# Kernel tuning notes

Hardware: AMD Instinct MI355X
Metric: run time of the kernel (lower is better)

## Reference

```python
import jax, jax.numpy as jnp
import numpy as np

BN_EPS = 1e-5


def gcn_conv(x, src, dst, n, W, b):
    # PyG GCNConv: h = x @ W; add self-loops; symmetric deg^{-1/2} norm; scatter-add; + bias
    h = x @ W
    sl = jnp.arange(n, dtype=src.dtype)
    src_f = jnp.concatenate([src, sl])
    dst_f = jnp.concatenate([dst, sl])
    deg = jax.ops.segment_sum(jnp.ones_like(dst_f, dtype=h.dtype), dst_f, num_segments=n)
    dis = jnp.where(deg > 0, jax.lax.rsqrt(jnp.maximum(deg, 1.0)), 0.0)
    norm = dis[src_f] * dis[dst_f]                       # [E+N]
    msg = h[src_f] * norm[:, None]                       # gather + scale
    out = jax.ops.segment_sum(msg, dst_f, num_segments=n)  # scatter-add
    return out + b


def batchnorm(x, g, b):
    # training-mode BatchNorm1d (batch statistics), deterministic
    mu = jnp.mean(x, axis=0)
    var = jnp.mean((x - mu) ** 2, axis=0)
    return g * (x - mu) * jax.lax.rsqrt(var + BN_EPS) + b


def setup_inputs() -> dict:
    key = jax.random.key(0)
    ks = jax.random.split(key, 12)
    N, E, F_IN, D, M, G = 40000, 640000, 128, 128, 256, 2000
    x = jax.random.normal(ks[0], (N, F_IN), dtype=jnp.float32)
    edge_index = jax.random.randint(ks[1], (2, E), 0, N, dtype=jnp.int64)
    batch = jnp.sort(jax.random.randint(ks[2], (N,), 0, G, dtype=jnp.int64))
    s = lambda fi: 1.0 / np.sqrt(fi)
    W1 = jax.random.normal(ks[3], (F_IN, D), dtype=jnp.float32) * s(F_IN)
    b1 = jnp.zeros((D,), jnp.float32)
    W2 = jax.random.normal(ks[4], (D, D), dtype=jnp.float32) * s(D)
    b2 = jnp.zeros((D,), jnp.float32)
    bn1_g = jnp.ones((D,), jnp.float32); bn1_b = jnp.zeros((D,), jnp.float32)
    bn2_g = jnp.ones((D,), jnp.float32); bn2_b = jnp.zeros((D,), jnp.float32)
    fc1_w = jax.random.normal(ks[5], (D, M), dtype=jnp.float32) * s(D)
    fc1_b = jnp.zeros((M,), jnp.float32)
    fc2_w = jax.random.normal(ks[6], (M, M), dtype=jnp.float32) * s(M)
    fc2_b = jnp.zeros((M,), jnp.float32)
    fc3_w = jax.random.normal(ks[7], (M, 1), dtype=jnp.float32) * s(M)
    fc3_b = jnp.zeros((1,), jnp.float32)
    return dict(x=x, edge_index=edge_index, batch=batch, num_graphs=G,
                W1=W1, b1=b1, W2=W2, b2=b2,
                bn1_g=bn1_g, bn1_b=bn1_b, bn2_g=bn2_g, bn2_b=bn2_b,
                fc1_w=fc1_w, fc1_b=fc1_b, fc2_w=fc2_w, fc2_b=fc2_b,
                fc3_w=fc3_w, fc3_b=fc3_b)


def reference(x, edge_index, batch, num_graphs, W1, b1, W2, b2,
              bn1_g, bn1_b, bn2_g, bn2_b,
              fc1_w, fc1_b, fc2_w, fc2_b, fc3_w, fc3_b):
    n = x.shape[0]
    src, dst = edge_index[0], edge_index[1]
    h = gcn_conv(x, src, dst, n, W1, b1)
    h = jax.nn.relu(batchnorm(h, bn1_g, bn1_b))
    h = gcn_conv(h, src, dst, n, W2, b2)
    h = jax.nn.relu(batchnorm(h, bn2_g, bn2_b))
    g = jax.ops.segment_sum(h, batch, num_segments=num_graphs)  # scatter_sum pooling [G, D]
    g = jax.nn.relu(g @ fc1_w + fc1_b)   # dropout is identity in eval
    g = jax.nn.relu(g @ fc2_w + fc2_b)
    return g @ fc3_w + fc3_b             # [G, 1]
```

## Files before the change

### kernel.cpp

```cpp
#include <hip/hip_runtime.h>
#include <hip/hip_fp16.h>

#define NN 40000
#define NE 640000
#define DF 128
#define NG 2000
#define NCH 157
#define CNTB 625
#define GT_BLKS 625
#define NDPAD 40192

typedef unsigned int u32;
typedef __attribute__((ext_vector_type(8))) short short8;
typedef __attribute__((ext_vector_type(4))) float floatx4;

__device__ inline float2 bf2_to_f2(u32 u) {
    return make_float2(__uint_as_float(u << 16), __uint_as_float(u & 0xffff0000u));
}
__device__ inline u32 f_to_bf(float f) {
    u32 u = __float_as_uint(f);
    return (u + 0x7fffu + ((u >> 16) & 1u)) >> 16;
}
__device__ inline u32 pack_bf2(float a, float b) {
    return f_to_bf(a) | (f_to_bf(b) << 16);
}
__device__ inline float bf_to_f(short s) {
    return __uint_as_float(((u32)(unsigned short)s) << 16);
}
__device__ inline float colw_to_f(int cw) {
    return __half2float(__ushort_as_half((unsigned short)((u32)cw >> 16)));
}

template<bool BF16IN, bool FUSE_BN>
__device__ __forceinline__ void gemm_core(const void* __restrict__ Xv, const unsigned short* __restrict__ wt,
                                          u32* __restrict__ outb, const float* __restrict__ slots,
                                          const float* __restrict__ gam, const float* __restrict__ bet,
                                          int bid, char* sbuf, float* sc, float* sh) {
    unsigned short* wlds = (unsigned short*)sbuf;
    unsigned short* clds = (unsigned short*)sbuf;
    int tid = threadIdx.x;
    int row0 = bid * 64;

    if (FUSE_BN) {
        if (tid < 128) {
            float s = 0.f, q = 0.f;
            for (int k = 0; k < 64; k++) {
                s += slots[k * 256 + tid];
                q += slots[k * 256 + 128 + tid];
            }
            const float inv_n = 1.0f / (float)NN;
            float mu = s * inv_n;
            float va = fmaf(-mu, mu, q * inv_n);
            float a = gam[tid] * rsqrtf(va + 1e-5f);
            sc[tid] = a;
            sh[tid] = fmaf(-mu, a, bet[tid]);
        }
    }
    for (int i = tid; i < 2048; i += 256) {
        int c = i >> 4, s = i & 15;
        *(uint4*)&wlds[c * 128 + ((s ^ (c & 7)) << 3)] = ((const uint4*)wt)[i];
    }
    __syncthreads();

    int lane = tid & 63;
    int wave = tid >> 6;
    int qr = lane >> 4;
    int rl = lane & 15;

    int rA = row0 + wave * 16 + rl;
    floatx4 acc[8];
#pragma unroll
    for (int b = 0; b < 8; b++) acc[b] = (floatx4){0.f, 0.f, 0.f, 0.f};
#pragma unroll
    for (int kb = 0; kb < 4; kb++) {
        int k0 = kb * 32 + qr * 8;
        short8 a0;
        if (!BF16IN) {
            const float* p0 = (const float*)Xv + (size_t)rA * DF + k0;
            float4 u0 = *(const float4*)p0, u1 = *(const float4*)(p0 + 4);
            float fa[8] = {u0.x, u0.y, u0.z, u0.w, u1.x, u1.y, u1.z, u1.w};
#pragma unroll
            for (int j = 0; j < 8; j++) a0[j] = (short)f_to_bf(fa[j]);
        } else {
            a0 = *(const short8*)((const u32*)Xv + (size_t)rA * 64 + (k0 >> 1));
            if (FUSE_BN) {
#pragma unroll
                for (int j = 0; j < 8; j++) {
                    float f0 = fmaxf(fmaf(bf_to_f(a0[j]), sc[k0 + j], sh[k0 + j]), 0.f);
                    a0[j] = (short)f_to_bf(f0);
                }
            }
        }
#pragma unroll
        for (int ct = 0; ct < 8; ct++) {
            int rowB = ct * 16 + rl;
            short8 bfr = *(const short8*)&wlds[rowB * 128 + ((((kb << 2) + qr) ^ (rl & 7)) << 3)];
            acc[ct] = __builtin_amdgcn_mfma_f32_16x16x32_bf16(a0, bfr, acc[ct], 0, 0, 0);
        }
    }
    __syncthreads();
#pragma unroll
    for (int ct = 0; ct < 8; ct++)
#pragma unroll
        for (int r = 0; r < 4; r++) {
            int lr = wave * 16 + qr * 4 + r;
            int c = ct * 16 + rl;
            clds[lr * 128 + (((c >> 3) ^ (lr & 7)) << 3) + (c & 7)] = (unsigned short)f_to_bf(acc[ct][r]);
        }
    __syncthreads();
    for (int i = tid; i < 1024; i += 256) {
        int lr = i >> 4, s = i & 15;
        uint4 v = *(const uint4*)&clds[lr * 128 + ((s ^ (lr & 7)) << 3)];
        ((uint4*)(outb + (size_t)(row0 + lr) * 64))[s] = v;
    }
}

__global__ __launch_bounds__(256) void k_prep(const float* __restrict__ W1, const float* __restrict__ W2,
                                              unsigned short* __restrict__ wt1, unsigned short* __restrict__ wt2,
                                              float* __restrict__ slots0, int* __restrict__ deg) {
    int bid = blockIdx.x, tid = threadIdx.x;
    if (bid < 64) {
        slots0[bid * 512 + tid] = 0.f;
        slots0[bid * 512 + 256 + tid] = 0.f;
    } else if (bid < 104) {
        int i = (bid - 64) * 1024 + tid;
#pragma unroll
        for (int q = 0; q < 4; q++) {
            int j = i + q * 256;
            if (j < NDPAD) deg[j] = 0;
        }
    } else if (bid < 168) {
        int i = (bid - 104) * 256 + tid;
        wt1[i] = (unsigned short)f_to_bf(W1[(i & 127) * 128 + (i >> 7)]);
    } else {
        int i = (bid - 168) * 256 + tid;
        wt2[i] = (unsigned short)f_to_bf(W2[(i & 127) * 128 + (i >> 7)]);
    }
}

__global__ __launch_bounds__(256, 5) void k_countgemm(const int* __restrict__ dst,
                                                      int* __restrict__ deg,
                                                      const unsigned short* __restrict__ wt1,
                                                      const float* __restrict__ X, u32* __restrict__ outb) {
    __shared__ __align__(16) char sbuf[32768];
    int bid = blockIdx.x;
    int tid = threadIdx.x;
    if (bid < CNTB) {
        int i4 = bid * 256 + tid;
        int4 d4 = ((const int4*)dst)[i4];
        atomicAdd(&deg[d4.x], 1);
        atomicAdd(&deg[d4.y], 1);
        atomicAdd(&deg[d4.z], 1);
        atomicAdd(&deg[d4.w], 1);
        return;
    }
    gemm_core<false, false>(X, wt1, outb, nullptr, nullptr, nullptr,
                            bid - CNTB, sbuf, nullptr, nullptr);
}

__global__ __launch_bounds__(256) void k_scan(const int* __restrict__ deg,
                                              int* __restrict__ row_ptr, int* __restrict__ curs,
                                              float* __restrict__ dis) {
    __shared__ int red[256];
    __shared__ int ls[256];
    int tid = threadIdx.x;
    int wnd = blockIdx.x;
    int part = 0;
    int lim = wnd * 256;
    for (int idx = tid; idx < lim; idx += 256) part += deg[idx];
    red[tid] = part;
    int n = lim + tid;
    int d = deg[n];
    ls[tid] = d;
    __syncthreads();
#pragma unroll
    for (int off = 128; off > 0; off >>= 1) {
        if (tid < off) red[tid] += red[tid + off];
        __syncthreads();
    }
    int base = red[0];
#pragma unroll
    for (int off = 1; off < 256; off <<= 1) {
        int t = (tid >= off) ? ls[tid - off] : 0;
        __syncthreads();
        ls[tid] += t;
        __syncthreads();
    }
    if (n < NN) {
        int r = base + ls[tid] - d;
        row_ptr[n] = r;
        curs[n] = r;
        dis[n] = rsqrtf((float)(d + 1));
    }
    if (wnd == NCH - 1 && tid == 0) row_ptr[NN] = NE;
}

__global__ __launch_bounds__(256) void k_fill(const int* __restrict__ src, const int* __restrict__ dst,
                                              int* __restrict__ curs,
                                              const float* __restrict__ dis, u32* __restrict__ col) {
    int i4 = blockIdx.x * 256 + threadIdx.x;
    int4 d4 = ((const int4*)dst)[i4];
    int4 s4 = ((const int4*)src)[i4];
    int dd[4] = {d4.x, d4.y, d4.z, d4.w};
    int ss[4] = {s4.x, s4.y, s4.z, s4.w};
#pragma unroll
    for (int q = 0; q < 4; q++) {
        u32 h = (u32)__half_as_ushort(__float2half(dis[ss[q]]));
        int slot = atomicAdd(&curs[dd[q]], 1);
        col[slot] = (u32)ss[q] | (h << 16);
    }
}

__global__ __launch_bounds__(256, 4) void k_gemm2(const u32* __restrict__ Hb, const unsigned short* __restrict__ wt2,
                                                  u32* __restrict__ outb, const float* __restrict__ slots,
                                                  const float* __restrict__ gam, const float* __restrict__ bet) {
    __shared__ __align__(16) char sbuf[32768];
    __shared__ float sc[128], sh[128];
    gemm_core<true, true>(Hb, wt2, outb, slots, gam, bet, blockIdx.x, sbuf, sc, sh);
}

__global__ __launch_bounds__(256, 8) void k_gather(const u32* __restrict__ Hb, const int* __restrict__ row_ptr,
                                                   const u32* __restrict__ col, const float* __restrict__ dis,
                                                   const float* __restrict__ bias, u32* __restrict__ outb,
                                                   float* __restrict__ slots) {
    __shared__ float sred[4][128];
    __shared__ float qred[4][128];
    int t = threadIdx.x & 63;
    int wv = threadIdx.x >> 6;
    int node = blockIdx.x * 4 + wv;
    float di = dis[node];
    int lo = row_ptr[node], hi = row_ptr[node + 1];
    float2 acc;
    {
        float2 a = bf2_to_f2(Hb[(size_t)node * 64 + t]);
        acc = make_float2(a.x * di, a.y * di);
    }
    for (int base = lo; base < hi; base += 64) {
        int m = hi - base; if (m > 64) m = 64;
        int cw = 0;
        if (t < m) cw = (int)col[base + t];
        int ng = (m + 3) >> 2;
        int c[4]; u32 u[4];
#pragma unroll
        for (int q = 0; q < 4; q++) {
            int idx = q < m ? q : 0;
            c[q] = __shfl(cw, idx);
            u[q] = Hb[(size_t)(c[q] & 0xffff) * 64 + t];
        }
        for (int g = 1; g < ng; g++) {
            int c2[4]; u32 u2[4];
#pragma unroll
            for (int q = 0; q < 4; q++) {
                int ii = g * 4 + q;
                int idx = ii < m ? ii : 0;
                c2[q] = __shfl(cw, idx);
                u2[q] = Hb[(size_t)(c2[q] & 0xffff) * 64 + t];
            }
#pragma unroll
            for (int q = 0; q < 4; q++) {
                int ii = (g - 1) * 4 + q;
                float wq = ii < m ? colw_to_f(c[q]) : 0.f;
                float2 h = bf2_to_f2(u[q]);
                acc.x = fmaf(h.x, wq, acc.x);
                acc.y = fmaf(h.y, wq, acc.y);
            }
#pragma unroll
            for (int q = 0; q < 4; q++) { c[q] = c2[q]; u[q] = u2[q]; }
        }
#pragma unroll
        for (int q = 0; q < 4; q++) {
            int ii = (ng - 1) * 4 + q;
            float wq = ii < m ? colw_to_f(c[q]) : 0.f;
            float2 h = bf2_to_f2(u[q]);
            acc.x = fmaf(h.x, wq, acc.x);
            acc.y = fmaf(h.y, wq, acc.y);
        }
    }
    float2 b = ((const float2*)bias)[t];
    acc.x = fmaf(acc.x, di, b.x);
    acc.y = fmaf(acc.y, di, b.y);
    outb[(size_t)node * 64 + t] = pack_bf2(acc.x, acc.y);
    sred[wv][2 * t] = acc.x;     sred[wv][2 * t + 1] = acc.y;
    qred[wv][2 * t] = acc.x * acc.x; qred[wv][2 * t + 1] = acc.y * acc.y;
    __syncthreads();
    int tid = threadIdx.x;
    if (tid < 128) {
        float s = sred[0][tid] + sred[1][tid] + sred[2][tid] + sred[3][tid];
        float q = qred[0][tid] + qred[1][tid] + qred[2][tid] + qred[3][tid];
        int slot = blockIdx.x & 63;
        atomicAdd(&slots[slot * 256 + tid], s);
        atomicAdd(&slots[slot * 256 + 128 + tid], q);
    }
}

__global__ __launch_bounds__(256) void k_poolfc(const u32* __restrict__ Hb, const int* __restrict__ batch,
                                                const float* __restrict__ slots,
                                                const float* __restrict__ gam, const float* __restrict__ bet,
                                                const float* __restrict__ fc1w, const float* __restrict__ fc1b,
                                                const float* __restrict__ fc2w, const float* __restrict__ fc2b,
                                                const float* __restrict__ fc3w, const float* __restrict__ fc3b,
                                                float* __restrict__ out) {
    __shared__ float sc[128], sh[128];
    __shared__ float pooled[4][128];
    __shared__ float g1[4][256];
    __shared__ float g2[4][256];
    __shared__ int bnds[5];
    int tid = threadIdx.x;
    int gbase = blockIdx.x * 4;
    if (tid < 128) {
        float s = 0.f, q = 0.f;
        for (int k = 0; k < 64; k++) {
            s += slots[k * 256 + tid];
            q += slots[k * 256 + 128 + tid];
        }
        const float inv_n = 1.0f / (float)NN;
        float mu = s * inv_n;
        float va = fmaf(-mu, mu, q * inv_n);
        float a = gam[tid] * rsqrtf(va + 1e-5f);
        sc[tid] = a;
        sh[tid] = fmaf(-mu, a, bet[tid]);
    } else if (tid < 133) {
        int target = gbase + (tid - 128);
        int a = 0, b = NN;
        while (a < b) { int m = (a + b) >> 1; if (batch[m] < target) a = m + 1; else b = m; }
        bnds[tid - 128] = a;
    }
    __syncthreads();
    {
        int g = tid >> 6, p = tid & 63;
        int lo = bnds[g], hi = bnds[g + 1];
        float a0 = 0.f, a1 = 0.f;
        float sc0 = sc[2 * p], sh0 = sh[2 * p], sc1 = sc[2 * p + 1], sh1 = sh[2 * p + 1];
        for (int i = lo; i < hi; i++) {
            float2 v = bf2_to_f2(Hb[(size_t)i * 64 + p]);
            a0 += fmaxf(fmaf(v.x, sc0, sh0), 0.f);
            a1 += fmaxf(fmaf(v.y, sc1, sh1), 0.f);
        }
        pooled[g][2 * p] = a0;
        pooled[g][2 * p + 1] = a1;
    }
    __syncthreads();
    {
        float x0 = 0.f, x1 = 0.f, x2 = 0.f, x3 = 0.f;
        for (int k = 0; k < 128; k++) {
            float wv = fc1w[k * 256 + tid];
            x0 = fmaf(pooled[0][k], wv, x0);
            x1 = fmaf(pooled[1][k], wv, x1);
            x2 = fmaf(pooled[2][k], wv, x2);
            x3 = fmaf(pooled[3][k], wv, x3);
        }
        float bb = fc1b[tid];
        g1[0][tid] = fmaxf(x0 + bb, 0.f);
        g1[1][tid] = fmaxf(x1 + bb, 0.f);
        g1[2][tid] = fmaxf(x2 + bb, 0.f);
        g1[3][tid] = fmaxf(x3 + bb, 0.f);
    }
    __syncthreads();
    {
        float x0 = 0.f, x1 = 0.f, x2 = 0.f, x3 = 0.f;
        for (int k = 0; k < 256; k++) {
            float wv = fc2w[k * 256 + tid];
            x0 = fmaf(g1[0][k], wv, x0);
            x1 = fmaf(g1[1][k], wv, x1);
            x2 = fmaf(g1[2][k], wv, x2);
            x3 = fmaf(g1[3][k], wv, x3);
        }
        float bb = fc2b[tid];
        g2[0][tid] = fmaxf(x0 + bb, 0.f);
        g2[1][tid] = fmaxf(x1 + bb, 0.f);
        g2[2][tid] = fmaxf(x2 + bb, 0.f);
        g2[3][tid] = fmaxf(x3 + bb, 0.f);
    }
    __syncthreads();
    {
        int lane = tid & 63, wv = tid >> 6;
        float s = fmaf(g2[wv][lane], fc3w[lane],
                  fmaf(g2[wv][64 + lane], fc3w[64 + lane],
                  fmaf(g2[wv][128 + lane], fc3w[128 + lane],
                       g2[wv][192 + lane] * fc3w[192 + lane])));
        for (int off = 32; off > 0; off >>= 1) s += __shfl_down(s, off);
        if (lane == 0) out[gbase + wv] = s + fc3b[0];
    }
}

extern "C" void kernel_launch(void* const* d_in, const int* in_sizes, int n_in,
                              void* d_out, int out_size, void* d_ws, size_t ws_size,
                              hipStream_t stream) {
    const float* x    = (const float*)d_in[0];
    const int*   ei   = (const int*)d_in[1];
    const int*   batch= (const int*)d_in[2];
    const float* W1   = (const float*)d_in[4];
    const float* b1   = (const float*)d_in[5];
    const float* W2   = (const float*)d_in[6];
    const float* b2   = (const float*)d_in[7];
    const float* bn1g = (const float*)d_in[8];
    const float* bn1b = (const float*)d_in[9];
    const float* bn2g = (const float*)d_in[10];
    const float* bn2b = (const float*)d_in[11];
    const float* fc1w = (const float*)d_in[12];
    const float* fc1b = (const float*)d_in[13];
    const float* fc2w = (const float*)d_in[14];
    const float* fc2b = (const float*)d_in[15];
    const float* fc3w = (const float*)d_in[16];
    const float* fc3b = (const float*)d_in[17];
    const int* src = ei;
    const int* dst = ei + NE;
    float* outp = (float*)d_out;

    char* w = (char*)d_ws;
    size_t o = 0;
    auto alloc = [&](size_t bytes) -> char* {
        char* p = w + o;
        o = (o + bytes + 255) & ~(size_t)255;
        return p;
    };
    int*   deg     = (int*)alloc((size_t)NDPAD * 4);
    int*   curs    = (int*)alloc((size_t)NDPAD * 4);
    float* slots0  = (float*)alloc((size_t)2 * 64 * 256 * 4);
    int*   row_ptr = (int*)alloc((size_t)(NN + 1) * 4);
    u32*   col     = (u32*)alloc((size_t)NE * 4);
    float* dis     = (float*)alloc((size_t)NN * 4);
    unsigned short* wt1 = (unsigned short*)alloc(128 * 128 * 2);
    unsigned short* wt2 = (unsigned short*)alloc(128 * 128 * 2);
    u32*   bufA    = (u32*)alloc((size_t)NN * 64 * 4);
    u32*   bufB    = (u32*)alloc((size_t)NN * 64 * 4);
    float* slotsA  = slots0;
    float* slotsB  = slots0 + 64 * 256;

    k_prep<<<232, 256, 0, stream>>>(W1, W2, wt1, wt2, slots0, deg);
    k_countgemm<<<CNTB + GT_BLKS, 256, 0, stream>>>(dst, deg, wt1, x, bufA);
    k_scan<<<NCH, 256, 0, stream>>>(deg, row_ptr, curs, dis);
    k_fill<<<CNTB, 256, 0, stream>>>(src, dst, curs, dis, col);
    k_gather<<<NN / 4, 256, 0, stream>>>(bufA, row_ptr, col, dis, b1, bufB, slotsA);
    k_gemm2<<<GT_BLKS, 256, 0, stream>>>(bufB, wt2, bufA, slotsA, bn1g, bn1b);
    k_gather<<<NN / 4, 256, 0, stream>>>(bufA, row_ptr, col, dis, b2, bufB, slotsB);
    k_poolfc<<<NG / 4, 256, 0, stream>>>(bufB, batch, slotsB, bn2g, bn2b,
                                         fc1w, fc1b, fc2w, fc2b, fc3w, fc3b, outp);
}
```

Before: 280.2 us.

## Build CSR with per-chunk LDS histograms and ranks instead of global atomics

Replaces the global-atomic degree count and cursor-based fill with a two-level counting sort. Each block builds a shared-memory histogram over one edge chunk and one node octant, and records per-edge ranks and per-window sums. The scan then computes per-chunk base offsets, so fill places each edge without atomics, deterministically. This removes global atomic contention, but adds large degT/baseT arrays (64×40960 ints) that are written and scanned, plus an 8x re-read of dst by the histogram blocks.

```diff
diff --git a/kernel.cpp b/kernel.cpp
--- a/kernel.cpp
+++ b/kernel.cpp
@@ -6,9 +6,15 @@
 #define DF 128
 #define NG 2000
 #define NCH 157
-#define CNTB 625
+#define FILLB 625
 #define GT_BLKS 625
-#define NDPAD 40192
+#define NCHUNK 64
+#define ECH 10000
+#define NOCT 8
+#define QN 5120
+#define NPAD (NOCT * QN)
+#define NWIN 160
+#define HISTB (NCHUNK * NOCT)
 
 typedef unsigned int u32;
 typedef __attribute__((ext_vector_type(8))) short short8;
@@ -117,60 +123,83 @@
 
 __global__ __launch_bounds__(256) void k_prep(const float* __restrict__ W1, const float* __restrict__ W2,
                                               unsigned short* __restrict__ wt1, unsigned short* __restrict__ wt2,
-                                              float* __restrict__ slots0, int* __restrict__ deg) {
+                                              float* __restrict__ slots0) {
     int bid = blockIdx.x, tid = threadIdx.x;
     if (bid < 64) {
         slots0[bid * 512 + tid] = 0.f;
         slots0[bid * 512 + 256 + tid] = 0.f;
-    } else if (bid < 104) {
-        int i = (bid - 64) * 1024 + tid;
-#pragma unroll
-        for (int q = 0; q < 4; q++) {
-            int j = i + q * 256;
-            if (j < NDPAD) deg[j] = 0;
-        }
-    } else if (bid < 168) {
-        int i = (bid - 104) * 256 + tid;
+    } else if (bid < 128) {
+        int i = (bid - 64) * 256 + tid;
         wt1[i] = (unsigned short)f_to_bf(W1[(i & 127) * 128 + (i >> 7)]);
     } else {
-        int i = (bid - 168) * 256 + tid;
+        int i = (bid - 128) * 256 + tid;
         wt2[i] = (unsigned short)f_to_bf(W2[(i & 127) * 128 + (i >> 7)]);
     }
 }
 
 __global__ __launch_bounds__(256, 5) void k_countgemm(const int* __restrict__ dst,
-                                                      int* __restrict__ deg,
+                                                      int* __restrict__ degT, int* __restrict__ rank,
+                                                      int* __restrict__ wsum,
                                                       const unsigned short* __restrict__ wt1,
                                                       const float* __restrict__ X, u32* __restrict__ outb) {
     __shared__ __align__(16) char sbuf[32768];
     int bid = blockIdx.x;
     int tid = threadIdx.x;
-    if (bid < CNTB) {
-        int i4 = bid * 256 + tid;
-        int4 d4 = ((const int4*)dst)[i4];
-        atomicAdd(&deg[d4.x], 1);
-        atomicAdd(&deg[d4.y], 1);
-        atomicAdd(&deg[d4.z], 1);
-        atomicAdd(&deg[d4.w], 1);
+    if (bid < HISTB) {
+        int c = bid >> 3, oct = bid & 7;
+        int nlo = oct * QN;
+        int* hist = (int*)sbuf;
+        for (int i = tid; i < QN; i += 256) hist[i] = 0;
+        __syncthreads();
+        int ebase = c * ECH;
+        const int4* dst4 = (const int4*)(dst + ebase);
+        for (int i4 = tid; i4 < 2500; i4 += 256) {
+            int4 d4 = dst4[i4];
+            int e = ebase + i4 * 4;
+            int t0 = d4.x - nlo, t1 = d4.y - nlo, t2 = d4.z - nlo, t3 = d4.w - nlo;
+            if ((u32)t0 < (u32)QN) rank[e]     = atomicAdd(&hist[t0], 1);
+            if ((u32)t1 < (u32)QN) rank[e + 1] = atomicAdd(&hist[t1], 1);
+            if ((u32)t2 < (u32)QN) rank[e + 2] = atomicAdd(&hist[t2], 1);
+            if ((u32)t3 < (u32)QN) rank[e + 3] = atomicAdd(&hist[t3], 1);
+        }
+        __syncthreads();
+        for (int i = tid; i < QN; i += 256) degT[(size_t)c * NPAD + nlo + i] = hist[i];
+        int wv = tid >> 6, lane = tid & 63;
+        for (int lw = wv; lw < 20; lw += 4) {
+            int v = hist[lw * 256 + lane] + hist[lw * 256 + 64 + lane]
+                  + hist[lw * 256 + 128 + lane] + hist[lw * 256 + 192 + lane];
+            for (int off = 32; off > 0; off >>= 1) v += __shfl_down(v, off);
+            if (lane == 0) wsum[c * NWIN + oct * 20 + lw] = v;
+        }
         return;
     }
     gemm_core<false, false>(X, wt1, outb, nullptr, nullptr, nullptr,
-                            bid - CNTB, sbuf, nullptr, nullptr);
-}
-
-__global__ __launch_bounds__(256) void k_scan(const int* __restrict__ deg,
-                                              int* __restrict__ row_ptr, int* __restrict__ curs,
-                                              float* __restrict__ dis) {
+                            bid - HISTB, sbuf, nullptr, nullptr);
+}
+
+__global__ __launch_bounds__(256) void k_scan(const int* __restrict__ degT, const int* __restrict__ wsum,
+                                              int* __restrict__ baseT,
+                                              int* __restrict__ row_ptr, float* __restrict__ dis) {
     __shared__ int red[256];
     __shared__ int ls[256];
     int tid = threadIdx.x;
     int wnd = blockIdx.x;
     int part = 0;
-    int lim = wnd * 256;
-    for (int idx = tid; idx < lim; idx += 256) part += deg[idx];
+    int wp = tid < NWIN ? tid : tid - NWIN;
+    for (int idx = tid; idx < NCHUNK * NWIN; idx += 256) {
+        if (wp < wnd) part += wsum[idx];
+        wp += 96; if (wp >= NWIN) wp -= NWIN;
+    }
     red[tid] = part;
-    int n = lim + tid;
-    int d = deg[n];
+    int n = wnd * 256 + tid;
+    int run = 0;
+#pragma unroll 4
+    for (int c = 0; c < NCHUNK; c++) {
+        int v = degT[(size_t)c * NPAD + n];
+        baseT[(size_t)c * NPAD + n] = run;
+        run += v;
+    }
+    int d = run;
     ls[tid] = d;
     __syncthreads();
 #pragma unroll
@@ -189,25 +218,28 @@
     if (n < NN) {
         int r = base + ls[tid] - d;
         row_ptr[n] = r;
-        curs[n] = r;
         dis[n] = rsqrtf((float)(d + 1));
     }
     if (wnd == NCH - 1 && tid == 0) row_ptr[NN] = NE;
 }
 
 __global__ __launch_bounds__(256) void k_fill(const int* __restrict__ src, const int* __restrict__ dst,
-                                              int* __restrict__ curs,
+                                              const int* __restrict__ rank, const int* __restrict__ row_ptr,
+                                              const int* __restrict__ baseT,
                                               const float* __restrict__ dis, u32* __restrict__ col) {
     int i4 = blockIdx.x * 256 + threadIdx.x;
     int4 d4 = ((const int4*)dst)[i4];
     int4 s4 = ((const int4*)src)[i4];
+    int4 r4 = ((const int4*)rank)[i4];
+    int e = i4 * 4;
     int dd[4] = {d4.x, d4.y, d4.z, d4.w};
     int ss[4] = {s4.x, s4.y, s4.z, s4.w};
+    int rr[4] = {r4.x, r4.y, r4.z, r4.w};
 #pragma unroll
     for (int q = 0; q < 4; q++) {
+        int c = (e + q) / ECH;
         u32 h = (u32)__half_as_ushort(__float2half(dis[ss[q]]));
-        int slot = atomicAdd(&curs[dd[q]], 1);
-        col[slot] = (u32)ss[q] | (h << 16);
+        col[row_ptr[dd[q]] + baseT[(size_t)c * NPAD + dd[q]] + rr[q]] = (u32)ss[q] | (h << 16);
     }
 }
 
@@ -414,10 +446,12 @@
         o = (o + bytes + 255) & ~(size_t)255;
         return p;
     };
-    int*   deg     = (int*)alloc((size_t)NDPAD * 4);
-    int*   curs    = (int*)alloc((size_t)NDPAD * 4);
+    int*   degT    = (int*)alloc((size_t)NCHUNK * NPAD * 4);
+    int*   baseT   = (int*)alloc((size_t)NCHUNK * NPAD * 4);
+    int*   wsum    = (int*)alloc((size_t)NCHUNK * NWIN * 4);
     float* slots0  = (float*)alloc((size_t)2 * 64 * 256 * 4);
     int*   row_ptr = (int*)alloc((size_t)(NN + 1) * 4);
+    int*   rank    = (int*)alloc((size_t)NE * 4);
     u32*   col     = (u32*)alloc((size_t)NE * 4);
     float* dis     = (float*)alloc((size_t)NN * 4);
     unsigned short* wt1 = (unsigned short*)alloc(128 * 128 * 2);
@@ -427,10 +461,10 @@
     float* slotsA  = slots0;
     float* slotsB  = slots0 + 64 * 256;
 
-    k_prep<<<232, 256, 0, stream>>>(W1, W2, wt1, wt2, slots0, deg);
-    k_countgemm<<<CNTB + GT_BLKS, 256, 0, stream>>>(dst, deg, wt1, x, bufA);
-    k_scan<<<NCH, 256, 0, stream>>>(deg, row_ptr, curs, dis);
-    k_fill<<<CNTB, 256, 0, stream>>>(src, dst, curs, dis, col);
+    k_prep<<<192, 256, 0, stream>>>(W1, W2, wt1, wt2, slots0);
+    k_countgemm<<<HISTB + GT_BLKS, 256, 0, stream>>>(dst, degT, rank, wsum, wt1, x, bufA);
+    k_scan<<<NCH, 256, 0, stream>>>(degT, wsum, baseT, row_ptr, dis);
+    k_fill<<<FILLB, 256, 0, stream>>>(src, dst, rank, row_ptr, baseT, dis, col);
     k_gather<<<NN / 4, 256, 0, stream>>>(bufA, row_ptr, col, dis, b1, bufB, slotsA);
     k_gemm2<<<GT_BLKS, 256, 0, stream>>>(bufB, wt2, bufA, slotsA, bn1g, bn1b);
     k_gather<<<NN / 4, 256, 0, stream>>>(bufA, row_ptr, col, dis, b2, bufB, slotsB);
```

Measured after the change: 247.2 us. 11.8% less time.
